# Performance work log

Measured on AMD Instinct MI355X. Metric: run time of the kernel, lower is better.

Reference implementation:

```python
import jax, jax.numpy as jnp
import numpy as np

N_NODES = 100000
HIDDEN = 64
IN_DIM = 64
NEG_SLOPE = 0.01  # torch LeakyReLU default


def setup_inputs() -> dict:
    key = jax.random.key(0)
    ks = jax.random.split(key, 8)
    x = jax.random.normal(ks[0], (N_NODES, IN_DIM), dtype=jnp.float32)
    edge_index = jax.random.randint(ks[1], (2, 1600000), 0, N_NODES, dtype=jnp.int64)
    # GCNConv weights: glorot-style scale, bias zero-init -> small randn for generality
    W1 = jax.random.normal(ks[2], (IN_DIM, HIDDEN), dtype=jnp.float32) / np.sqrt(IN_DIM)
    W2 = jax.random.normal(ks[3], (HIDDEN, HIDDEN), dtype=jnp.float32) / np.sqrt(HIDDEN)
    W3 = jax.random.normal(ks[4], (HIDDEN, HIDDEN), dtype=jnp.float32) / np.sqrt(HIDDEN)
    b1 = jax.random.normal(ks[5], (HIDDEN,), dtype=jnp.float32) * 0.01
    b2 = jax.random.normal(ks[6], (HIDDEN,), dtype=jnp.float32) * 0.01
    b3 = jax.random.normal(ks[7], (HIDDEN,), dtype=jnp.float32) * 0.01
    return {"x": x, "edge_index": edge_index, "W1": W1, "b1": b1,
            "W2": W2, "b2": b2, "W3": W3, "b3": b3}


def _gcn_graph(edge_index, n_nodes):
    # Add self loops (PyG GCNConv default) and compute symmetric normalization.
    src = jnp.concatenate([edge_index[0], jnp.arange(n_nodes, dtype=edge_index.dtype)])
    dst = jnp.concatenate([edge_index[1], jnp.arange(n_nodes, dtype=edge_index.dtype)])
    deg = jax.ops.segment_sum(jnp.ones_like(dst, dtype=jnp.float32), dst,
                              num_segments=n_nodes)
    dinv = jax.lax.rsqrt(deg)  # deg >= 1 due to self loops
    norm = dinv[src] * dinv[dst]  # [E+N]
    return src, dst, norm


def _gcn_layer(h, W, b, src, dst, norm, n_nodes):
    h = h @ W  # linear first (PyG order), small GEMM
    agg = jax.ops.segment_sum(h[src] * norm[:, None], dst, num_segments=n_nodes)
    return agg + b


def reference(x, edge_index, W1, b1, W2, b2, W3, b3):
    n = x.shape[0]
    src, dst, norm = _gcn_graph(edge_index, n)
    lrelu = lambda v: jnp.where(v >= 0, v, NEG_SLOPE * v)
    h = lrelu(_gcn_layer(x, W1, b1, src, dst, norm, n))
    h = lrelu(_gcn_layer(h, W2, b2, src, dst, norm, n))
    h = lrelu(_gcn_layer(h, W3, b3, src, dst, norm, n))
    return h  # dropout is identity in eval mode
```

## Files before the change

### kernel.cpp

```cpp
#include <hip/hip_runtime.h>
#include <hip/hip_fp16.h>

#define HID 64
#define NEG_SLOPE 0.01f
#define BSHIFT 7
#define BWIDTH 128
#define MAXBUCK 1024
#define BCH 6144
#define NCH 512

__device__ __forceinline__ float4 h4load(const uint2* __restrict__ Hp, long long idx) {
    uint2 r = Hp[idx];
    __half2 a = *reinterpret_cast<__half2*>(&r.x);
    __half2 b = *reinterpret_cast<__half2*>(&r.y);
    float2 lo = __half22float2(a);
    float2 hi = __half22float2(b);
    return make_float4(lo.x, lo.y, hi.x, hi.y);
}

__device__ __forceinline__ uint2 h4pack(float4 v) {
    __half2 a = __floats2half2_rn(v.x, v.y);
    __half2 b = __floats2half2_rn(v.z, v.w);
    uint2 r;
    r.x = *reinterpret_cast<unsigned int*>(&a);
    r.y = *reinterpret_cast<unsigned int*>(&b);
    return r;
}

__global__ void f2h_kernel(const float4* __restrict__ in, uint2* __restrict__ out, int n4) {
    int i = blockIdx.x * 256 + threadIdx.x;
    if (i < n4) out[i] = h4pack(in[i]);
}

__global__ void detect_dtype_kernel(const unsigned int* __restrict__ e, int* __restrict__ flag) {
    __shared__ int nz;
    if (threadIdx.x == 0) nz = 0;
    __syncthreads();
    unsigned int v = e[2 * threadIdx.x + 1];
    if (v != 0u) atomicAdd(&nz, 1);
    __syncthreads();
    if (threadIdx.x == 0) *flag = (nz == 0) ? 1 : 0;
}

__device__ __forceinline__ long long edge_at(const void* e, long long idx, int is64) {
    if (is64) return ((const long long*)e)[idx];
    return (long long)((const int*)e)[idx];
}

__global__ void bhist_kernel(const void* __restrict__ edges, const int* __restrict__ flag,
                             unsigned int* __restrict__ bhist, long long E, int nbuck) {
    __shared__ unsigned int h[MAXBUCK];
    int t = threadIdx.x;
    for (int i = t; i < nbuck; i += 256) h[i] = 0;
    __syncthreads();
    int is64 = *flag;
    for (long long i = (long long)blockIdx.x * blockDim.x + t; i < E;
         i += (long long)gridDim.x * blockDim.x) {
        int d = (int)edge_at(edges, E + i, is64);
        atomicAdd(&h[d >> BSHIFT], 1u);
    }
    __syncthreads();
    for (int i = t; i < nbuck; i += 256)
        if (h[i]) atomicAdd(&bhist[i], h[i]);
}

__global__ void bscan_kernel(const unsigned int* __restrict__ bhist,
                             unsigned int* __restrict__ bbase,
                             unsigned int* __restrict__ bcursor, int nbuck) {
    __shared__ unsigned int s[512];
    __shared__ unsigned int carry;
    int t = threadIdx.x;
    if (t == 0) carry = 0;
    __syncthreads();
    for (int base = 0; base < nbuck; base += 512) {
        int i = base + t;
        unsigned int v = (i < nbuck) ? bhist[i] : 0u;
        s[t] = v;
        __syncthreads();
        for (int off = 1; off < 512; off <<= 1) {
            unsigned int tv = (t >= off) ? s[t - off] : 0u;
            __syncthreads();
            s[t] += tv;
            __syncthreads();
        }
        unsigned int total = s[511];
        if (i < nbuck) {
            bbase[i] = s[t] - v + carry;
            bcursor[i] = s[t] - v + carry;
        }
        __syncthreads();
        if (t == 0) carry += total;
        __syncthreads();
    }
}

__global__ __launch_bounds__(512) void bin_kernel(const void* __restrict__ edges,
                                                  const int* __restrict__ flag,
                                                  unsigned int* __restrict__ bcursor,
                                                  int2* __restrict__ bbuf, long long E, int nbuck) {
    __shared__ unsigned int lcnt[MAXBUCK], lbase[MAXBUCK], loff[MAXBUCK];
    int t = threadIdx.x;
    for (int i = t; i < nbuck; i += 512) lcnt[i] = 0;
    __syncthreads();
    long long base = (long long)blockIdx.x * BCH;
    long long lim = base + BCH < E ? base + BCH : E;
    int is64 = *flag;
    for (long long i = base + t; i < lim; i += 512) {
        int d = (int)edge_at(edges, E + i, is64);
        atomicAdd(&lcnt[d >> BSHIFT], 1u);
    }
    __syncthreads();
    for (int i = t; i < nbuck; i += 512) {
        if (lcnt[i]) lbase[i] = atomicAdd(&bcursor[i], lcnt[i]);
        loff[i] = 0;
    }
    __syncthreads();
    for (long long i = base + t; i < lim; i += 512) {
        int s = (int)edge_at(edges, i, is64);
        int d = (int)edge_at(edges, E + i, is64);
        int b = d >> BSHIFT;
        unsigned int pos = lbase[b] + atomicAdd(&loff[b], 1u);
        bbuf[pos] = make_int2(s, d);
    }
}

__global__ __launch_bounds__(256) void bdeg_kernel(const int2* __restrict__ bbuf,
                                                   const unsigned int* __restrict__ bbase,
                                                   const unsigned int* __restrict__ bhist,
                                                   unsigned int* __restrict__ deg,
                                                   unsigned int* __restrict__ dhist, int n) {
    __shared__ unsigned int h[BWIDTH];
    __shared__ unsigned int dh[256];
    int t = threadIdx.x;
    int b = blockIdx.x;
    if (t < BWIDTH) h[t] = 0;
    dh[t] = 0;
    __syncthreads();
    unsigned int s0 = bbase[b], cnt = bhist[b];
    int lo = b << BSHIFT;
    for (unsigned int i = s0 + t; i < s0 + cnt; i += 256)
        atomicAdd(&h[bbuf[i].y - lo], 1u);
    __syncthreads();
    if (t < BWIDTH) {
        int node = lo + t;
        if (node < n) {
            unsigned int d = h[t];
            deg[node] = d;
            atomicAdd(&dh[d > 255u ? 255u : d], 1u);
        }
    }
    __syncthreads();
    if (dh[t]) atomicAdd(&dhist[t], dh[t]);
}

__global__ void scan1_kernel(const unsigned int* __restrict__ deg, int n,
                             unsigned int* __restrict__ offs, unsigned int* __restrict__ bsum) {
    __shared__ unsigned int s[256];
    int t = threadIdx.x;
    int i = blockIdx.x * 256 + t;
    unsigned int v = (i < n) ? deg[i] : 0u;
    s[t] = v;
    __syncthreads();
    for (int off = 1; off < 256; off <<= 1) {
        unsigned int tv = (t >= off) ? s[t - off] : 0u;
        __syncthreads();
        s[t] += tv;
        __syncthreads();
    }
    if (i < n) offs[i] = s[t] - v;
    if (t == 255) bsum[blockIdx.x] = s[255];
}

__global__ void scan2_kernel(unsigned int* __restrict__ bsum, int nb) {
    __shared__ unsigned int s[512];
    __shared__ unsigned int carry;
    int t = threadIdx.x;
    if (t == 0) carry = 0;
    __syncthreads();
    for (int base = 0; base < nb; base += 512) {
        int i = base + t;
        unsigned int v = (i < nb) ? bsum[i] : 0u;
        s[t] = v;
        __syncthreads();
        for (int off = 1; off < 512; off <<= 1) {
            unsigned int tv = (t >= off) ? s[t - off] : 0u;
            __syncthreads();
            s[t] += tv;
            __syncthreads();
        }
        unsigned int total = s[511];
        if (i < nb) bsum[i] = s[t] - v + carry;
        __syncthreads();
        if (t == 0) carry += total;
        __syncthreads();
    }
}

__global__ void scan3_kernel(unsigned int* __restrict__ offs, const unsigned int* __restrict__ bsum,
                             const unsigned int* __restrict__ deg, float* __restrict__ dinv,
                             unsigned int* __restrict__ ends, int n) {
    int i = blockIdx.x * 256 + threadIdx.x;
    if (i >= n) return;
    unsigned int o = offs[i] + bsum[blockIdx.x];
    offs[i] = o;
    ends[i] = o + deg[i];
    dinv[i] = rsqrtf((float)deg[i] + 1.0f);
}

__global__ void dscan_kernel(const unsigned int* __restrict__ dhist,
                             unsigned int* __restrict__ dcur) {
    __shared__ unsigned int s[256];
    int t = threadIdx.x;
    unsigned int v = dhist[t];
    s[t] = v;
    __syncthreads();
    for (int off = 1; off < 256; off <<= 1) {
        unsigned int tv = (t >= off) ? s[t - off] : 0u;
        __syncthreads();
        s[t] += tv;
        __syncthreads();
    }
    dcur[t] = s[t] - v;
}

__global__ __launch_bounds__(256) void dplace_kernel(const unsigned int* __restrict__ deg,
                                                     unsigned int* __restrict__ dcur,
                                                     unsigned int* __restrict__ perm, int n) {
    __shared__ unsigned int lcnt[256], lbase[256], loff[256];
    int t = threadIdx.x;
    lcnt[t] = 0;
    __syncthreads();
    int base = blockIdx.x * NCH;
    int lim = base + NCH < n ? base + NCH : n;
    for (int i = base + t; i < lim; i += 256) {
        unsigned int d = deg[i];
        atomicAdd(&lcnt[d > 255u ? 255u : d], 1u);
    }
    __syncthreads();
    if (lcnt[t]) lbase[t] = atomicAdd(&dcur[t], lcnt[t]);
    loff[t] = 0;
    __syncthreads();
    for (int i = base + t; i < lim; i += 256) {
        unsigned int d = deg[i];
        unsigned int b = d > 255u ? 255u : d;
        unsigned int pos = lbase[b] + atomicAdd(&loff[b], 1u);
        perm[pos] = (unsigned int)i;
    }
}

__global__ __launch_bounds__(256) void fill2_kernel(const int2* __restrict__ bbuf,
                                                    const unsigned int* __restrict__ bbase,
                                                    const unsigned int* __restrict__ bhist,
                                                    const unsigned int* __restrict__ offs,
                                                    const float* __restrict__ dinv,
                                                    int2* __restrict__ csr, int n) {
    __shared__ unsigned int cur[BWIDTH];
    __shared__ float dl[BWIDTH];
    int t = threadIdx.x;
    int b = blockIdx.x;
    int lo = b << BSHIFT;
    if (t < BWIDTH) {
        int node = lo + t;
        if (node < n) {
            cur[t] = offs[node];
            dl[t] = dinv[node];
        }
    }
    __syncthreads();
    unsigned int s0 = bbase[b], cnt = bhist[b];
    for (unsigned int i = s0 + t; i < s0 + cnt; i += 256) {
        int2 e = bbuf[i];
        int dloc = e.y - lo;
        unsigned int pos = atomicAdd(&cur[dloc], 1u);
        csr[pos] = make_int2(e.x, __float_as_int(dinv[e.x] * dl[dloc]));
    }
}

__global__ __launch_bounds__(256) void fused_layer_kernel(
        const int2* __restrict__ csr,
        const unsigned int* __restrict__ offs, const unsigned int* __restrict__ endo,
        const unsigned int* __restrict__ perm,
        const float* __restrict__ dinv, const uint2* __restrict__ h,
        const float* __restrict__ W, const float* __restrict__ b,
        float* __restrict__ outf, uint2* __restrict__ outh, int n, int ngroups) {
    __shared__ float Ws[64 * 64];

    int tid = threadIdx.x;
    int ln = tid >> 4;
    int part = tid & 15;
    for (int i = tid; i < 1024; i += 256)
        ((float4*)Ws)[i] = ((const float4*)W)[i];
    __syncthreads();

    __shared__ float aggs[16][72];
    float4 bb = ((const float4*)b)[part];

    for (int g = blockIdx.x; g < ngroups; g += gridDim.x) {
        int grp = ngroups - 1 - g;
        int idx = grp * 16 + ln;
        bool pred = idx < n;
        int node = pred ? (int)perm[idx] : 0;

        float4 a0 = make_float4(0.f, 0.f, 0.f, 0.f);
        float4 a1 = a0, a2 = a0, a3 = a0, a4 = a0, a5 = a0, a6 = a0, a7 = a0;
        if (pred) {
            unsigned int e = offs[node];
            unsigned int end = endo[node];
            for (; e + 8 <= end; e += 8) {
                int2 p0 = csr[e];     int2 p1 = csr[e + 1];
                int2 p2 = csr[e + 2]; int2 p3 = csr[e + 3];
                int2 p4 = csr[e + 4]; int2 p5 = csr[e + 5];
                int2 p6 = csr[e + 6]; int2 p7 = csr[e + 7];
                float4 v0 = h4load(h, (long long)p0.x * 16 + part);
                float4 v1 = h4load(h, (long long)p1.x * 16 + part);
                float4 v2 = h4load(h, (long long)p2.x * 16 + part);
                float4 v3 = h4load(h, (long long)p3.x * 16 + part);
                float4 v4 = h4load(h, (long long)p4.x * 16 + part);
                float4 v5 = h4load(h, (long long)p5.x * 16 + part);
                float4 v6 = h4load(h, (long long)p6.x * 16 + part);
                float4 v7 = h4load(h, (long long)p7.x * 16 + part);
                float w0 = __int_as_float(p0.y); float w1 = __int_as_float(p1.y);
                float w2 = __int_as_float(p2.y); float w3 = __int_as_float(p3.y);
                float w4 = __int_as_float(p4.y); float w5 = __int_as_float(p5.y);
                float w6 = __int_as_float(p6.y); float w7 = __int_as_float(p7.y);
                a0.x = fmaf(w0, v0.x, a0.x); a0.y = fmaf(w0, v0.y, a0.y);
                a0.z = fmaf(w0, v0.z, a0.z); a0.w = fmaf(w0, v0.w, a0.w);
                a1.x = fmaf(w1, v1.x, a1.x); a1.y = fmaf(w1, v1.y, a1.y);
                a1.z = fmaf(w1, v1.z, a1.z); a1.w = fmaf(w1, v1.w, a1.w);
                a2.x = fmaf(w2, v2.x, a2.x); a2.y = fmaf(w2, v2.y, a2.y);
                a2.z = fmaf(w2, v2.z, a2.z); a2.w = fmaf(w2, v2.w, a2.w);
                a3.x = fmaf(w3, v3.x, a3.x); a3.y = fmaf(w3, v3.y, a3.y);
                a3.z = fmaf(w3, v3.z, a3.z); a3.w = fmaf(w3, v3.w, a3.w);
                a4.x = fmaf(w4, v4.x, a4.x); a4.y = fmaf(w4, v4.y, a4.y);
                a4.z = fmaf(w4, v4.z, a4.z); a4.w = fmaf(w4, v4.w, a4.w);
                a5.x = fmaf(w5, v5.x, a5.x); a5.y = fmaf(w5, v5.y, a5.y);
                a5.z = fmaf(w5, v5.z, a5.z); a5.w = fmaf(w5, v5.w, a5.w);
                a6.x = fmaf(w6, v6.x, a6.x); a6.y = fmaf(w6, v6.y, a6.y);
                a6.z = fmaf(w6, v6.z, a6.z); a6.w = fmaf(w6, v6.w, a6.w);
                a7.x = fmaf(w7, v7.x, a7.x); a7.y = fmaf(w7, v7.y, a7.y);
                a7.z = fmaf(w7, v7.z, a7.z); a7.w = fmaf(w7, v7.w, a7.w);
            }
            if (e + 4 <= end) {
                int2 p0 = csr[e];     int2 p1 = csr[e + 1];
                int2 p2 = csr[e + 2]; int2 p3 = csr[e + 3];
                float4 v0 = h4load(h, (long long)p0.x * 16 + part);
                float4 v1 = h4load(h, (long long)p1.x * 16 + part);
                float4 v2 = h4load(h, (long long)p2.x * 16 + part);
                float4 v3 = h4load(h, (long long)p3.x * 16 + part);
                float w0 = __int_as_float(p0.y); float w1 = __int_as_float(p1.y);
                float w2 = __int_as_float(p2.y); float w3 = __int_as_float(p3.y);
                a0.x = fmaf(w0, v0.x, a0.x); a0.y = fmaf(w0, v0.y, a0.y);
                a0.z = fmaf(w0, v0.z, a0.z); a0.w = fmaf(w0, v0.w, a0.w);
                a1.x = fmaf(w1, v1.x, a1.x); a1.y = fmaf(w1, v1.y, a1.y);
                a1.z = fmaf(w1, v1.z, a1.z); a1.w = fmaf(w1, v1.w, a1.w);
                a2.x = fmaf(w2, v2.x, a2.x); a2.y = fmaf(w2, v2.y, a2.y);
                a2.z = fmaf(w2, v2.z, a2.z); a2.w = fmaf(w2, v2.w, a2.w);
                a3.x = fmaf(w3, v3.x, a3.x); a3.y = fmaf(w3, v3.y, a3.y);
                a3.z = fmaf(w3, v3.z, a3.z); a3.w = fmaf(w3, v3.w, a3.w);
                e += 4;
            }
            for (; e < end; ++e) {
                int2 p0 = csr[e];
                float4 v0 = h4load(h, (long long)p0.x * 16 + part);
                float w0 = __int_as_float(p0.y);
                a0.x = fmaf(w0, v0.x, a0.x); a0.y = fmaf(w0, v0.y, a0.y);
                a0.z = fmaf(w0, v0.z, a0.z); a0.w = fmaf(w0, v0.w, a0.w);
            }
            float dv = dinv[node];
            float d2 = dv * dv;
            float4 a = h4load(h, (long long)node * 16 + part);
            a0.x = fmaf(d2, a.x, ((a0.x + a1.x) + (a2.x + a3.x)) + ((a4.x + a5.x) + (a6.x + a7.x)));
            a0.y = fmaf(d2, a.y, ((a0.y + a1.y) + (a2.y + a3.y)) + ((a4.y + a5.y) + (a6.y + a7.y)));
            a0.z = fmaf(d2, a.z, ((a0.z + a1.z) + (a2.z + a3.z)) + ((a4.z + a5.z) + (a6.z + a7.z)));
            a0.w = fmaf(d2, a.w, ((a0.w + a1.w) + (a2.w + a3.w)) + ((a4.w + a5.w) + (a6.w + a7.w)));
            *(float4*)&aggs[ln][part * 4] = a0;

            float4 o = bb;
#pragma unroll 8
            for (int k = 0; k < 64; ++k) {
                float av = aggs[ln][k];
                float4 w = *(const float4*)&Ws[k * 64 + part * 4];
                o.x = fmaf(av, w.x, o.x);
                o.y = fmaf(av, w.y, o.y);
                o.z = fmaf(av, w.z, o.z);
                o.w = fmaf(av, w.w, o.w);
            }
            o.x = (o.x >= 0.f) ? o.x : NEG_SLOPE * o.x;
            o.y = (o.y >= 0.f) ? o.y : NEG_SLOPE * o.y;
            o.z = (o.z >= 0.f) ? o.z : NEG_SLOPE * o.z;
            o.w = (o.w >= 0.f) ? o.w : NEG_SLOPE * o.w;
            long long oidx = (long long)node * 16 + part;
            if (outh) outh[oidx] = h4pack(o);
            else ((float4*)outf)[oidx] = o;
        }
    }
}

extern "C" void kernel_launch(void* const* d_in, const int* in_sizes, int n_in,
                              void* d_out, int out_size, void* d_ws, size_t ws_size,
                              hipStream_t stream) {
    const float* x  = (const float*)d_in[0];
    const void*  edges = d_in[1];
    const float* W1 = (const float*)d_in[2];
    const float* b1 = (const float*)d_in[3];
    const float* W2 = (const float*)d_in[4];
    const float* b2 = (const float*)d_in[5];
    const float* W3 = (const float*)d_in[6];
    const float* b3 = (const float*)d_in[7];
    float* out = (float*)d_out;

    const long long E = (long long)in_sizes[1] / 2;
    const int n = in_sizes[0] / HID;
    const int nb = (n + 255) / 256;
    const int nbuck = (n + BWIDTH - 1) >> BSHIFT;

    char* ws = (char*)d_ws;
    size_t off = 0;
    auto alloc = [&](size_t bytes) {
        char* p = ws + off;
        off += (bytes + 255) & ~(size_t)255;
        return p;
    };
    int* flag            = (int*)alloc(256);
    unsigned int* deg    = (unsigned int*)alloc((size_t)n * 4);
    float* dinv          = (float*)alloc((size_t)n * 4);
    unsigned int* offs   = (unsigned int*)alloc((size_t)n * 4);
    unsigned int* ends   = (unsigned int*)alloc((size_t)n * 4);
    unsigned int* perm   = (unsigned int*)alloc((size_t)n * 4);
    unsigned int* bsum   = (unsigned int*)alloc((size_t)nb * 4);
    unsigned int* bhist  = (unsigned int*)alloc(MAXBUCK * 4);
    unsigned int* bbase  = (unsigned int*)alloc(MAXBUCK * 4);
    unsigned int* bcur   = (unsigned int*)alloc(MAXBUCK * 4);
    unsigned int* dhist  = (unsigned int*)alloc(256 * 4);
    unsigned int* dcur   = (unsigned int*)alloc(256 * 4);
    int2* csr            = (int2*)alloc((size_t)E * 8);
    uint2* X16           = (uint2*)alloc((size_t)n * HID * 2);
    uint2* Hh1           = (uint2*)alloc((size_t)n * HID * 2);
    uint2* Hh2           = (uint2*)alloc((size_t)n * HID * 2);
    int2* bbuf           = (int2*)alloc((size_t)E * 8);

    detect_dtype_kernel<<<1, 256, 0, stream>>>((const unsigned int*)edges, flag);
    hipMemsetAsync(bhist, 0, MAXBUCK * 4, stream);
    hipMemsetAsync(dhist, 0, 256 * 4, stream);
    f2h_kernel<<<(n * 16 + 255) / 256, 256, 0, stream>>>((const float4*)x, X16, n * 16);
    bhist_kernel<<<1024, 256, 0, stream>>>(edges, flag, bhist, E, nbuck);
    bscan_kernel<<<1, 512, 0, stream>>>(bhist, bbase, bcur, nbuck);
    bin_kernel<<<(int)((E + BCH - 1) / BCH), 512, 0, stream>>>(edges, flag, bcur, bbuf, E, nbuck);
    bdeg_kernel<<<nbuck, 256, 0, stream>>>(bbuf, bbase, bhist, deg, dhist, n);
    dscan_kernel<<<1, 256, 0, stream>>>(dhist, dcur);
    dplace_kernel<<<(n + NCH - 1) / NCH, 256, 0, stream>>>(deg, dcur, perm, n);
    scan1_kernel<<<nb, 256, 0, stream>>>(deg, n, offs, bsum);
    scan2_kernel<<<1, 512, 0, stream>>>(bsum, nb);
    scan3_kernel<<<nb, 256, 0, stream>>>(offs, bsum, deg, dinv, ends, n);
    fill2_kernel<<<nbuck, 256, 0, stream>>>(bbuf, bbase, bhist, offs, dinv, csr, n);

    const int ngroups = (n + 15) / 16;
    const int pgrid = 256 * 7;
    fused_layer_kernel<<<pgrid, 256, 0, stream>>>(csr, offs, ends, perm, dinv, X16, W1, b1,
                                                  nullptr, Hh1, n, ngroups);
    fused_layer_kernel<<<pgrid, 256, 0, stream>>>(csr, offs, ends, perm, dinv, Hh1, W2, b2,
                                                  nullptr, Hh2, n, ngroups);
    fused_layer_kernel<<<pgrid, 256, 0, stream>>>(csr, offs, ends, perm, dinv, Hh2, W3, b3,
                                                  out, nullptr, n, ngroups);
}
```

Measured before the change: 340.7 us.

## Widen gather to 16-byte loads, merge scans into bucket kernel, drop memsets

The layer kernel now uses 8 threads per node, each loading 16-byte half8 chunks, so a block covers 32 nodes. The edge loop is unrolled by 12 into 4 accumulator pairs, and the grid is resized. The three-kernel global scan is replaced by a per-bucket local scan inside the degree kernel, using bucket bases already computed. The two memsets are folded into the dtype-detect kernel. Together these aim to cut launch count and make the gather transactions wider, at the cost of more registers per thread.

Result: faster. 307.0 us (-9.9%).

```diff
diff --git a/kernel.cpp b/kernel.cpp
--- a/kernel.cpp
+++ b/kernel.cpp
@@ -9,13 +9,49 @@
 #define BCH 6144
 #define NCH 512
 
-__device__ __forceinline__ float4 h4load(const uint2* __restrict__ Hp, long long idx) {
-    uint2 r = Hp[idx];
+__device__ __forceinline__ void h8load(const uint4* __restrict__ Hp, long long idx,
+                                       float4& lo, float4& hi) {
+    uint4 r = Hp[idx];
     __half2 a = *reinterpret_cast<__half2*>(&r.x);
     __half2 b = *reinterpret_cast<__half2*>(&r.y);
-    float2 lo = __half22float2(a);
-    float2 hi = __half22float2(b);
-    return make_float4(lo.x, lo.y, hi.x, hi.y);
+    __half2 c = *reinterpret_cast<__half2*>(&r.z);
+    __half2 d = *reinterpret_cast<__half2*>(&r.w);
+    float2 f0 = __half22float2(a), f1 = __half22float2(b);
+    float2 f2 = __half22float2(c), f3 = __half22float2(d);
+    lo = make_float4(f0.x, f0.y, f1.x, f1.y);
+    hi = make_float4(f2.x, f2.y, f3.x, f3.y);
+}
+
+__device__ __forceinline__ void cvt8(uint4 r, float4& lo, float4& hi) {
+    __half2 a = *reinterpret_cast<__half2*>(&r.x);
+    __half2 b = *reinterpret_cast<__half2*>(&r.y);
+    __half2 c = *reinterpret_cast<__half2*>(&r.z);
+    __half2 d = *reinterpret_cast<__half2*>(&r.w);
+    float2 f0 = __half22float2(a), f1 = __half22float2(b);
+    float2 f2 = __half22float2(c), f3 = __half22float2(d);
+    lo = make_float4(f0.x, f0.y, f1.x, f1.y);
+    hi = make_float4(f2.x, f2.y, f3.x, f3.y);
+}
+
+__device__ __forceinline__ void fma8(float wt, const float4& lo, const float4& hi,
+                                     float4& al, float4& ah) {
+    al.x = fmaf(wt, lo.x, al.x); al.y = fmaf(wt, lo.y, al.y);
+    al.z = fmaf(wt, lo.z, al.z); al.w = fmaf(wt, lo.w, al.w);
+    ah.x = fmaf(wt, hi.x, ah.x); ah.y = fmaf(wt, hi.y, ah.y);
+    ah.z = fmaf(wt, hi.z, ah.z); ah.w = fmaf(wt, hi.w, ah.w);
+}
+
+__device__ __forceinline__ uint4 h8pack(float4 lo, float4 hi) {
+    __half2 a = __floats2half2_rn(lo.x, lo.y);
+    __half2 b = __floats2half2_rn(lo.z, lo.w);
+    __half2 c = __floats2half2_rn(hi.x, hi.y);
+    __half2 d = __floats2half2_rn(hi.z, hi.w);
+    uint4 r;
+    r.x = *reinterpret_cast<unsigned int*>(&a);
+    r.y = *reinterpret_cast<unsigned int*>(&b);
+    r.z = *reinterpret_cast<unsigned int*>(&c);
+    r.w = *reinterpret_cast<unsigned int*>(&d);
+    return r;
 }
 
 __device__ __forceinline__ uint2 h4pack(float4 v) {
@@ -32,14 +68,19 @@
     if (i < n4) out[i] = h4pack(in[i]);
 }
 
-__global__ void detect_dtype_kernel(const unsigned int* __restrict__ e, int* __restrict__ flag) {
+__global__ void detect_dtype_kernel(const unsigned int* __restrict__ e, int* __restrict__ flag,
+                                    unsigned int* __restrict__ bhist,
+                                    unsigned int* __restrict__ dhist) {
     __shared__ int nz;
-    if (threadIdx.x == 0) nz = 0;
-    __syncthreads();
-    unsigned int v = e[2 * threadIdx.x + 1];
+    int t = threadIdx.x;
+    if (t == 0) nz = 0;
+    __syncthreads();
+    unsigned int v = e[2 * t + 1];
     if (v != 0u) atomicAdd(&nz, 1);
-    __syncthreads();
-    if (threadIdx.x == 0) *flag = (nz == 0) ? 1 : 0;
+    for (int i = t; i < MAXBUCK; i += 256) bhist[i] = 0;
+    dhist[t] = 0;
+    __syncthreads();
+    if (t == 0) *flag = (nz == 0) ? 1 : 0;
 }
 
 __device__ __forceinline__ long long edge_at(const void* e, long long idx, int is64) {
@@ -124,12 +165,16 @@
     }
 }
 
-__global__ __launch_bounds__(256) void bdeg_kernel(const int2* __restrict__ bbuf,
-                                                   const unsigned int* __restrict__ bbase,
-                                                   const unsigned int* __restrict__ bhist,
-                                                   unsigned int* __restrict__ deg,
-                                                   unsigned int* __restrict__ dhist, int n) {
+__global__ __launch_bounds__(256) void mergeA_kernel(const int2* __restrict__ bbuf,
+                                                     const unsigned int* __restrict__ bbase,
+                                                     const unsigned int* __restrict__ bhist,
+                                                     unsigned int* __restrict__ deg,
+                                                     float* __restrict__ dinv,
+                                                     unsigned int* __restrict__ offs,
+                                                     unsigned int* __restrict__ ends,
+                                                     unsigned int* __restrict__ dhist, int n) {
     __shared__ unsigned int h[BWIDTH];
+    __shared__ unsigned int sc[BWIDTH];
     __shared__ unsigned int dh[256];
     int t = threadIdx.x;
     int b = blockIdx.x;
@@ -141,70 +186,28 @@
     for (unsigned int i = s0 + t; i < s0 + cnt; i += 256)
         atomicAdd(&h[bbuf[i].y - lo], 1u);
     __syncthreads();
+    if (t < BWIDTH) sc[t] = h[t];
+    __syncthreads();
+    for (int off = 1; off < BWIDTH; off <<= 1) {
+        unsigned int v = (t < BWIDTH && t >= off) ? sc[t - off] : 0u;
+        __syncthreads();
+        if (t < BWIDTH) sc[t] += v;
+        __syncthreads();
+    }
     if (t < BWIDTH) {
         int node = lo + t;
         if (node < n) {
             unsigned int d = h[t];
+            unsigned int o = s0 + sc[t] - d;
             deg[node] = d;
+            offs[node] = o;
+            ends[node] = o + d;
+            dinv[node] = rsqrtf((float)d + 1.0f);
             atomicAdd(&dh[d > 255u ? 255u : d], 1u);
         }
     }
     __syncthreads();
     if (dh[t]) atomicAdd(&dhist[t], dh[t]);
-}
-
-__global__ void scan1_kernel(const unsigned int* __restrict__ deg, int n,
-                             unsigned int* __restrict__ offs, unsigned int* __restrict__ bsum) {
-    __shared__ unsigned int s[256];
-    int t = threadIdx.x;
-    int i = blockIdx.x * 256 + t;
-    unsigned int v = (i < n) ? deg[i] : 0u;
-    s[t] = v;
-    __syncthreads();
-    for (int off = 1; off < 256; off <<= 1) {
-        unsigned int tv = (t >= off) ? s[t - off] : 0u;
-        __syncthreads();
-        s[t] += tv;
-        __syncthreads();
-    }
-    if (i < n) offs[i] = s[t] - v;
-    if (t == 255) bsum[blockIdx.x] = s[255];
-}
-
-__global__ void scan2_kernel(unsigned int* __restrict__ bsum, int nb) {
-    __shared__ unsigned int s[512];
-    __shared__ unsigned int carry;
-    int t = threadIdx.x;
-    if (t == 0) carry = 0;
-    __syncthreads();
-    for (int base = 0; base < nb; base += 512) {
-        int i = base + t;
-        unsigned int v = (i < nb) ? bsum[i] : 0u;
-        s[t] = v;
-        __syncthreads();
-        for (int off = 1; off < 512; off <<= 1) {
-            unsigned int tv = (t >= off) ? s[t - off] : 0u;
-            __syncthreads();
-            s[t] += tv;
-            __syncthreads();
-        }
-        unsigned int total = s[511];
-        if (i < nb) bsum[i] = s[t] - v + carry;
-        __syncthreads();
-        if (t == 0) carry += total;
-        __syncthreads();
-    }
-}
-
-__global__ void scan3_kernel(unsigned int* __restrict__ offs, const unsigned int* __restrict__ bsum,
-                             const unsigned int* __restrict__ deg, float* __restrict__ dinv,
-                             unsigned int* __restrict__ ends, int n) {
-    int i = blockIdx.x * 256 + threadIdx.x;
-    if (i >= n) return;
-    unsigned int o = offs[i] + bsum[blockIdx.x];
-    offs[i] = o;
-    ends[i] = o + deg[i];
-    dinv[i] = rsqrtf((float)deg[i] + 1.0f);
 }
 
 __global__ void dscan_kernel(const unsigned int* __restrict__ dhist,
@@ -280,118 +283,112 @@
         const int2* __restrict__ csr,
         const unsigned int* __restrict__ offs, const unsigned int* __restrict__ endo,
         const unsigned int* __restrict__ perm,
-        const float* __restrict__ dinv, const uint2* __restrict__ h,
+        const float* __restrict__ dinv, const uint4* __restrict__ h,
         const float* __restrict__ W, const float* __restrict__ b,
-        float* __restrict__ outf, uint2* __restrict__ outh, int n, int ngroups) {
+        float* __restrict__ outf, uint4* __restrict__ outh, int n, int ngroups) {
     __shared__ float Ws[64 * 64];
+    __shared__ float aggs[32][66];
 
     int tid = threadIdx.x;
-    int ln = tid >> 4;
-    int part = tid & 15;
+    int ln = tid >> 3;
+    int p8 = tid & 7;
     for (int i = tid; i < 1024; i += 256)
         ((float4*)Ws)[i] = ((const float4*)W)[i];
     __syncthreads();
 
-    __shared__ float aggs[16][72];
-    float4 bb = ((const float4*)b)[part];
+    float4 bb0 = ((const float4*)b)[p8 * 2];
+    float4 bb1 = ((const float4*)b)[p8 * 2 + 1];
 
     for (int g = blockIdx.x; g < ngroups; g += gridDim.x) {
         int grp = ngroups - 1 - g;
-        int idx = grp * 16 + ln;
+        int idx = grp * 32 + ln;
         bool pred = idx < n;
         int node = pred ? (int)perm[idx] : 0;
 
-        float4 a0 = make_float4(0.f, 0.f, 0.f, 0.f);
-        float4 a1 = a0, a2 = a0, a3 = a0, a4 = a0, a5 = a0, a6 = a0, a7 = a0;
+        float4 Al[4], Ah[4];
+#pragma unroll
+        for (int s = 0; s < 4; ++s) {
+            Al[s] = make_float4(0.f, 0.f, 0.f, 0.f);
+            Ah[s] = make_float4(0.f, 0.f, 0.f, 0.f);
+        }
         if (pred) {
             unsigned int e = offs[node];
             unsigned int end = endo[node];
-            for (; e + 8 <= end; e += 8) {
-                int2 p0 = csr[e];     int2 p1 = csr[e + 1];
-                int2 p2 = csr[e + 2]; int2 p3 = csr[e + 3];
-                int2 p4 = csr[e + 4]; int2 p5 = csr[e + 5];
-                int2 p6 = csr[e + 6]; int2 p7 = csr[e + 7];
-                float4 v0 = h4load(h, (long long)p0.x * 16 + part);
-                float4 v1 = h4load(h, (long long)p1.x * 16 + part);
-                float4 v2 = h4load(h, (long long)p2.x * 16 + part);
-                float4 v3 = h4load(h, (long long)p3.x * 16 + part);
-                float4 v4 = h4load(h, (long long)p4.x * 16 + part);
-                float4 v5 = h4load(h, (long long)p5.x * 16 + part);
-                float4 v6 = h4load(h, (long long)p6.x * 16 + part);
-                float4 v7 = h4load(h, (long long)p7.x * 16 + part);
-                float w0 = __int_as_float(p0.y); float w1 = __int_as_float(p1.y);
-                float w2 = __int_as_float(p2.y); float w3 = __int_as_float(p3.y);
-                float w4 = __int_as_float(p4.y); float w5 = __int_as_float(p5.y);
-                float w6 = __int_as_float(p6.y); float w7 = __int_as_float(p7.y);
-                a0.x = fmaf(w0, v0.x, a0.x); a0.y = fmaf(w0, v0.y, a0.y);
-                a0.z = fmaf(w0, v0.z, a0.z); a0.w = fmaf(w0, v0.w, a0.w);
-                a1.x = fmaf(w1, v1.x, a1.x); a1.y = fmaf(w1, v1.y, a1.y);
-                a1.z = fmaf(w1, v1.z, a1.z); a1.w = fmaf(w1, v1.w, a1.w);
-                a2.x = fmaf(w2, v2.x, a2.x); a2.y = fmaf(w2, v2.y, a2.y);
-                a2.z = fmaf(w2, v2.z, a2.z); a2.w = fmaf(w2, v2.w, a2.w);
-                a3.x = fmaf(w3, v3.x, a3.x); a3.y = fmaf(w3, v3.y, a3.y);
-                a3.z = fmaf(w3, v3.z, a3.z); a3.w = fmaf(w3, v3.w, a3.w);
-                a4.x = fmaf(w4, v4.x, a4.x); a4.y = fmaf(w4, v4.y, a4.y);
-                a4.z = fmaf(w4, v4.z, a4.z); a4.w = fmaf(w4, v4.w, a4.w);
-                a5.x = fmaf(w5, v5.x, a5.x); a5.y = fmaf(w5, v5.y, a5.y);
-                a5.z = fmaf(w5, v5.z, a5.z); a5.w = fmaf(w5, v5.w, a5.w);
-                a6.x = fmaf(w6, v6.x, a6.x); a6.y = fmaf(w6, v6.y, a6.y);
-                a6.z = fmaf(w6, v6.z, a6.z); a6.w = fmaf(w6, v6.w, a6.w);
-                a7.x = fmaf(w7, v7.x, a7.x); a7.y = fmaf(w7, v7.y, a7.y);
-                a7.z = fmaf(w7, v7.z, a7.z); a7.w = fmaf(w7, v7.w, a7.w);
+            for (; e + 12 <= end; e += 12) {
+                int2 pp[12];
+#pragma unroll
+                for (int j = 0; j < 12; ++j) pp[j] = csr[e + j];
+                uint4 rr[12];
+#pragma unroll
+                for (int j = 0; j < 12; ++j) rr[j] = h[(long long)pp[j].x * 8 + p8];
+#pragma unroll
+                for (int j = 0; j < 12; ++j) {
+                    float4 lo, hi;
+                    cvt8(rr[j], lo, hi);
+                    fma8(__int_as_float(pp[j].y), lo, hi, Al[j & 3], Ah[j & 3]);
+                }
             }
-            if (e + 4 <= end) {
-                int2 p0 = csr[e];     int2 p1 = csr[e + 1];
-                int2 p2 = csr[e + 2]; int2 p3 = csr[e + 3];
-                float4 v0 = h4load(h, (long long)p0.x * 16 + part);
-                float4 v1 = h4load(h, (long long)p1.x * 16 + part);
-                float4 v2 = h4load(h, (long long)p2.x * 16 + part);
-                float4 v3 = h4load(h, (long long)p3.x * 16 + part);
-                float w0 = __int_as_float(p0.y); float w1 = __int_as_float(p1.y);
-                float w2 = __int_as_float(p2.y); float w3 = __int_as_float(p3.y);
-                a0.x = fmaf(w0, v0.x, a0.x); a0.y = fmaf(w0, v0.y, a0.y);
-                a0.z = fmaf(w0, v0.z, a0.z); a0.w = fmaf(w0, v0.w, a0.w);
-                a1.x = fmaf(w1, v1.x, a1.x); a1.y = fmaf(w1, v1.y, a1.y);
-                a1.z = fmaf(w1, v1.z, a1.z); a1.w = fmaf(w1, v1.w, a1.w);
-                a2.x = fmaf(w2, v2.x, a2.x); a2.y = fmaf(w2, v2.y, a2.y);
-                a2.z = fmaf(w2, v2.z, a2.z); a2.w = fmaf(w2, v2.w, a2.w);
-                a3.x = fmaf(w3, v3.x, a3.x); a3.y = fmaf(w3, v3.y, a3.y);
-                a3.z = fmaf(w3, v3.z, a3.z); a3.w = fmaf(w3, v3.w, a3.w);
-                e += 4;
+            for (; e + 4 <= end; e += 4) {
+                int2 pp[4];
+#pragma unroll
+                for (int j = 0; j < 4; ++j) pp[j] = csr[e + j];
+                uint4 rr[4];
+#pragma unroll
+                for (int j = 0; j < 4; ++j) rr[j] = h[(long long)pp[j].x * 8 + p8];
+#pragma unroll
+                for (int j = 0; j < 4; ++j) {
+                    float4 lo, hi;
+                    cvt8(rr[j], lo, hi);
+                    fma8(__int_as_float(pp[j].y), lo, hi, Al[j], Ah[j]);
+                }
             }
             for (; e < end; ++e) {
                 int2 p0 = csr[e];
-                float4 v0 = h4load(h, (long long)p0.x * 16 + part);
-                float w0 = __int_as_float(p0.y);
-                a0.x = fmaf(w0, v0.x, a0.x); a0.y = fmaf(w0, v0.y, a0.y);
-                a0.z = fmaf(w0, v0.z, a0.z); a0.w = fmaf(w0, v0.w, a0.w);
+                float4 lo, hi;
+                h8load(h, (long long)p0.x * 8 + p8, lo, hi);
+                fma8(__int_as_float(p0.y), lo, hi, Al[0], Ah[0]);
             }
             float dv = dinv[node];
             float d2 = dv * dv;
-            float4 a = h4load(h, (long long)node * 16 + part);
-            a0.x = fmaf(d2, a.x, ((a0.x + a1.x) + (a2.x + a3.x)) + ((a4.x + a5.x) + (a6.x + a7.x)));
-            a0.y = fmaf(d2, a.y, ((a0.y + a1.y) + (a2.y + a3.y)) + ((a4.y + a5.y) + (a6.y + a7.y)));
-            a0.z = fmaf(d2, a.z, ((a0.z + a1.z) + (a2.z + a3.z)) + ((a4.z + a5.z) + (a6.z + a7.z)));
-            a0.w = fmaf(d2, a.w, ((a0.w + a1.w) + (a2.w + a3.w)) + ((a4.w + a5.w) + (a6.w + a7.w)));
-            *(float4*)&aggs[ln][part * 4] = a0;
-
-            float4 o = bb;
+            float4 slo, shi;
+            h8load(h, (long long)node * 8 + p8, slo, shi);
+            float4 fl, fh;
+            fl.x = fmaf(d2, slo.x, (Al[0].x + Al[1].x) + (Al[2].x + Al[3].x));
+            fl.y = fmaf(d2, slo.y, (Al[0].y + Al[1].y) + (Al[2].y + Al[3].y));
+            fl.z = fmaf(d2, slo.z, (Al[0].z + Al[1].z) + (Al[2].z + Al[3].z));
+            fl.w = fmaf(d2, slo.w, (Al[0].w + Al[1].w) + (Al[2].w + Al[3].w));
+            fh.x = fmaf(d2, shi.x, (Ah[0].x + Ah[1].x) + (Ah[2].x + Ah[3].x));
+            fh.y = fmaf(d2, shi.y, (Ah[0].y + Ah[1].y) + (Ah[2].y + Ah[3].y));
+            fh.z = fmaf(d2, shi.z, (Ah[0].z + Ah[1].z) + (Ah[2].z + Ah[3].z));
+            fh.w = fmaf(d2, shi.w, (Ah[0].w + Ah[1].w) + (Ah[2].w + Ah[3].w));
+            *(float4*)&aggs[ln][p8 * 8] = fl;
+            *(float4*)&aggs[ln][p8 * 8 + 4] = fh;
+
+            float4 o0 = bb0, o1 = bb1;
 #pragma unroll 8
             for (int k = 0; k < 64; ++k) {
                 float av = aggs[ln][k];
-                float4 w = *(const float4*)&Ws[k * 64 + part * 4];
-                o.x = fmaf(av, w.x, o.x);
-                o.y = fmaf(av, w.y, o.y);
-                o.z = fmaf(av, w.z, o.z);
-                o.w = fmaf(av, w.w, o.w);
+                float4 w0 = *(const float4*)&Ws[k * 64 + p8 * 8];
+                float4 w1 = *(const float4*)&Ws[k * 64 + p8 * 8 + 4];
+                o0.x = fmaf(av, w0.x, o0.x); o0.y = fmaf(av, w0.y, o0.y);
+                o0.z = fmaf(av, w0.z, o0.z); o0.w = fmaf(av, w0.w, o0.w);
+                o1.x = fmaf(av, w1.x, o1.x); o1.y = fmaf(av, w1.y, o1.y);
+                o1.z = fmaf(av, w1.z, o1.z); o1.w = fmaf(av, w1.w, o1.w);
             }
-            o.x = (o.x >= 0.f) ? o.x : NEG_SLOPE * o.x;
-            o.y = (o.y >= 0.f) ? o.y : NEG_SLOPE * o.y;
-            o.z = (o.z >= 0.f) ? o.z : NEG_SLOPE * o.z;
-            o.w = (o.w >= 0.f) ? o.w : NEG_SLOPE * o.w;
-            long long oidx = (long long)node * 16 + part;
-            if (outh) outh[oidx] = h4pack(o);
-            else ((float4*)outf)[oidx] = o;
+            o0.x = (o0.x >= 0.f) ? o0.x : NEG_SLOPE * o0.x;
+            o0.y = (o0.y >= 0.f) ? o0.y : NEG_SLOPE * o0.y;
+            o0.z = (o0.z >= 0.f) ? o0.z : NEG_SLOPE * o0.z;
+            o0.w = (o0.w >= 0.f) ? o0.w : NEG_SLOPE * o0.w;
+            o1.x = (o1.x >= 0.f) ? o1.x : NEG_SLOPE * o1.x;
+            o1.y = (o1.y >= 0.f) ? o1.y : NEG_SLOPE * o1.y;
+            o1.z = (o1.z >= 0.f) ? o1.z : NEG_SLOPE * o1.z;
+            o1.w = (o1.w >= 0.f) ? o1.w : NEG_SLOPE * o1.w;
+            if (outh) {
+                outh[(long long)node * 8 + p8] = h8pack(o0, o1);
+            } else {
+                ((float4*)outf)[(long long)node * 16 + p8 * 2] = o0;
+                ((float4*)outf)[(long long)node * 16 + p8 * 2 + 1] = o1;
+            }
         }
     }
 }
@@ -411,7 +408,6 @@
 
     const long long E = (long long)in_sizes[1] / 2;
     const int n = in_sizes[0] / HID;
-    const int nb = (n + 255) / 256;
     const int nbuck = (n + BWIDTH - 1) >> BSHIFT;
 
     char* ws = (char*)d_ws;
@@ -427,35 +423,29 @@
     unsigned int* offs   = (unsigned int*)alloc((size_t)n * 4);
     unsigned int* ends   = (unsigned int*)alloc((size_t)n * 4);
     unsigned int* perm   = (unsigned int*)alloc((size_t)n * 4);
-    unsigned int* bsum   = (unsigned int*)alloc((size_t)nb * 4);
     unsigned int* bhist  = (unsigned int*)alloc(MAXBUCK * 4);
     unsigned int* bbase  = (unsigned int*)alloc(MAXBUCK * 4);
     unsigned int* bcur   = (unsigned int*)alloc(MAXBUCK * 4);
     unsigned int* dhist  = (unsigned int*)alloc(256 * 4);
     unsigned int* dcur   = (unsigned int*)alloc(256 * 4);
     int2* csr            = (int2*)alloc((size_t)E * 8);
-    uint2* X16           = (uint2*)alloc((size_t)n * HID * 2);
-    uint2* Hh1           = (uint2*)alloc((size_t)n * HID * 2);
-    uint2* Hh2           = (uint2*)alloc((size_t)n * HID * 2);
+    uint4* X16           = (uint4*)alloc((size_t)n * HID * 2);
+    uint4* Hh1           = (uint4*)alloc((size_t)n * HID * 2);
+    uint4* Hh2           = (uint4*)alloc((size_t)n * HID * 2);
     int2* bbuf           = (int2*)alloc((size_t)E * 8);
 
-    detect_dtype_kernel<<<1, 256, 0, stream>>>((const unsigned int*)edges, flag);
-    hipMemsetAsync(bhist, 0, MAXBUCK * 4, stream);
-    hipMemsetAsync(dhist, 0, 256 * 4, stream);
-    f2h_kernel<<<(n * 16 + 255) / 256, 256, 0, stream>>>((const float4*)x, X16, n * 16);
+    detect_dtype_kernel<<<1, 256, 0, stream>>>((const unsigned int*)edges, flag, bhist, dhist);
+    f2h_kernel<<<(n * 16 + 255) / 256, 256, 0, stream>>>((const float4*)x, (uint2*)X16, n * 16);
     bhist_kernel<<<1024, 256, 0, stream>>>(edges, flag, bhist, E, nbuck);
     bscan_kernel<<<1, 512, 0, stream>>>(bhist, bbase, bcur, nbuck);
     bin_kernel<<<(int)((E + BCH - 1) / BCH), 512, 0, stream>>>(edges, flag, bcur, bbuf, E, nbuck);
-    bdeg_kernel<<<nbuck, 256, 0, stream>>>(bbuf, bbase, bhist, deg, dhist, n);
+    mergeA_kernel<<<nbuck, 256, 0, stream>>>(bbuf, bbase, bhist, deg, dinv, offs, ends, dhist, n);
     dscan_kernel<<<1, 256, 0, stream>>>(dhist, dcur);
     dplace_kernel<<<(n + NCH - 1) / NCH, 256, 0, stream>>>(deg, dcur, perm, n);
-    scan1_kernel<<<nb, 256, 0, stream>>>(deg, n, offs, bsum);
-    scan2_kernel<<<1, 512, 0, stream>>>(bsum, nb);
-    scan3_kernel<<<nb, 256, 0, stream>>>(offs, bsum, deg, dinv, ends, n);
     fill2_kernel<<<nbuck, 256, 0, stream>>>(bbuf, bbase, bhist, offs, dinv, csr, n);
 
-    const int ngroups = (n + 15) / 16;
-    const int pgrid = 256 * 7;
+    const int ngroups = (n + 31) / 32;
+    const int pgrid = 1024;
     fused_layer_kernel<<<pgrid, 256, 0, stream>>>(csr, offs, ends, perm, dinv, X16, W1, b1,
                                                   nullptr, Hh1, n, ngroups);
     fused_layer_kernel<<<pgrid, 256, 0, stream>>>(csr, offs, ends, perm, dinv, Hh1, W2, b2,
```
